# Kernel tuning notes

Hardware: AMD Instinct MI355X
Metric: run time of the kernel (lower is better)

## Reference

```python
import jax, jax.numpy as jnp
import numpy as np

HIDDEN = 768
NUM_HEADS = 12
HEAD_SIZE = HIDDEN // NUM_HEADS
LN_EPS = 1e-12


def setup_inputs() -> dict:
    key = jax.random.key(0)
    ks = jax.random.split(key, 10)
    B, S, H = 32, 512, HIDDEN
    std = 1.0 / np.sqrt(H)
    inp = {
        "x": jax.random.normal(ks[0], (B, S, H), dtype=jnp.float32),
        "additive_attention_mask": jnp.zeros((B, 1, 1, S), dtype=jnp.float32),
        "Wq": jax.random.normal(ks[1], (H, H), dtype=jnp.float32) * std,
        "bq": jax.random.normal(ks[2], (H,), dtype=jnp.float32) * 0.02,
        "Wk": jax.random.normal(ks[3], (H, H), dtype=jnp.float32) * std,
        "bk": jax.random.normal(ks[4], (H,), dtype=jnp.float32) * 0.02,
        "Wv": jax.random.normal(ks[5], (H, H), dtype=jnp.float32) * std,
        "bv": jax.random.normal(ks[6], (H,), dtype=jnp.float32) * 0.02,
        "Wo": jax.random.normal(ks[7], (H, H), dtype=jnp.float32) * std,
        "bo": jax.random.normal(ks[8], (H,), dtype=jnp.float32) * 0.02,
        "ln_w": jnp.ones((H,), dtype=jnp.float32),
        "ln_b": jnp.zeros((H,), dtype=jnp.float32),
    }
    return inp


def _split_heads(y):
    # (b, s, h) -> (b, n_heads, s, head_size)
    b, s, _ = y.shape
    return y.reshape(b, s, NUM_HEADS, HEAD_SIZE).transpose(0, 2, 1, 3)


def reference(x, additive_attention_mask, Wq, bq, Wk, bk, Wv, bv, Wo, bo, ln_w, ln_b):
    # Linear projections (torch Linear: x @ W.T + b)
    q = _split_heads(x @ Wq.T + bq)  # b n s d
    k = _split_heads(x @ Wk.T + bk)
    v = _split_heads(x @ Wv.T + bv)

    scores = jnp.einsum("bnqd,bnkd->bnqk", q, k) / np.sqrt(HEAD_SIZE)
    scores = scores + additive_attention_mask  # (b,1,1,s) broadcasts
    attn = jax.nn.softmax(scores, axis=-1)

    weighted = jnp.einsum("bnqk,bnkd->bnqd", attn, v)
    b, n, s, d = weighted.shape
    weighted = weighted.transpose(0, 2, 1, 3).reshape(b, s, n * d)
    attn_out = weighted @ Wo.T + bo

    # residual + LayerNorm (dropout is identity in eval)
    y = x + attn_out
    mean = jnp.mean(y, axis=-1, keepdims=True)
    var = jnp.var(y, axis=-1, keepdims=True)
    y = (y - mean) / jnp.sqrt(var + LN_EPS)
    return y * ln_w + ln_b
```

## Files before the change

kernel.cpp:

```cpp
#include <hip/hip_runtime.h>

#define HIDDEN 768
#define NHEAD 12
#define HDIM 64
#define SEQ 512
#define BATCH 32
#define MTOT (BATCH*SEQ)

typedef __attribute__((ext_vector_type(8))) short short8;
typedef __attribute__((ext_vector_type(4))) float f32x4;
typedef __attribute__((ext_vector_type(4))) unsigned short us4;

#define LOG2E 1.44269504088896340736f

__device__ __forceinline__ unsigned short f2bf(float f){
  unsigned u = __builtin_bit_cast(unsigned, f);
  u += 0x7fff + ((u >> 16) & 1);
  return (unsigned short)(u >> 16);
}

__device__ __forceinline__ float bf2f(unsigned short s){
  unsigned u = ((unsigned)s) << 16;
  return __builtin_bit_cast(float, u);
}

__device__ __forceinline__ float fexp2(float x){
  float r;
  asm("v_exp_f32 %0, %1\n\ts_nop 0" : "=v"(r) : "v"(x));
  return r;
}

__device__ __forceinline__ void gload16(unsigned short* lds, const unsigned short* g){
  __builtin_amdgcn_global_load_lds(
      (const __attribute__((address_space(1))) void*)g,
      (__attribute__((address_space(3))) void*)lds, 16, 0, 0);
}

__global__ __launch_bounds__(256) void cvt_kernel(const float* __restrict__ in,
                                                  unsigned short* __restrict__ out, int n4){
  int i = blockIdx.x * blockDim.x + threadIdx.x;
  if (i >= n4) return;
  float4 v = ((const float4*)in)[i];
  ushort4 o;
  o.x = f2bf(v.x); o.y = f2bf(v.y); o.z = f2bf(v.z); o.w = f2bf(v.w);
  ((ushort4*)out)[i] = o;
}

__global__ __launch_bounds__(256) void cvt4_kernel(
    const float* __restrict__ w0, const float* __restrict__ w1,
    const float* __restrict__ w2, const float* __restrict__ w3,
    unsigned short* __restrict__ o0, unsigned short* __restrict__ o1,
    unsigned short* __restrict__ o2, unsigned short* __restrict__ o3){
  const int which = blockIdx.y;
  const float* in = (which==0)?w0:((which==1)?w1:((which==2)?w2:w3));
  unsigned short* out = (which==0)?o0:((which==1)?o1:((which==2)?o2:o3));
  int i = blockIdx.x * blockDim.x + threadIdx.x;
  float4 v = ((const float4*)in)[i];
  ushort4 o;
  o.x = f2bf(v.x); o.y = f2bf(v.y); o.z = f2bf(v.z); o.w = f2bf(v.w);
  ((ushort4*)out)[i] = o;
}


#define STAGE_A(buf, kt_) do { \
    const int kc_ = (kt_)*64; \
    gload16(&sA[buf][(size_t)(tid)*8],      gA + kc_); \
    gload16(&sA[buf][(size_t)(512+tid)*8],  gA + (size_t)64*HIDDEN + kc_); \
    gload16(&sA[buf][(size_t)(1024+tid)*8], gA + (size_t)128*HIDDEN + kc_); \
    gload16(&sA[buf][(size_t)(1536+tid)*8], gA + (size_t)192*HIDDEN + kc_); \
  } while(0)

#define STAGE_B(buf, kt_) do { \
    const int kc_ = (kt_)*64; \
    gload16(&sB[buf][(size_t)(tid)*8],      gB + kc_); \
    gload16(&sB[buf][(size_t)(512+tid)*8],  gB + (size_t)64*HIDDEN + kc_); \
    gload16(&sB[buf][(size_t)(1024+tid)*8], gB + (size_t)128*HIDDEN + kc_); \
  } while(0)

#define GEMM_MAIN() \
  STAGE_A(0, 0); STAGE_B(0, 0); \
  for (int kt = 0; kt < 12; ++kt) { \
    const int c = kt & 1; \
    asm volatile("s_waitcnt vmcnt(0)" ::: "memory"); \
    __builtin_amdgcn_s_barrier(); \
    if (kt < 11) { STAGE_A(c^1, kt+1); STAGE_B(c^1, kt+1); } \
    const unsigned short* bA = sA[c]; \
    const unsigned short* bB = sB[c]; \
    _Pragma("unroll") \
    for (int kk = 0; kk < 2; ++kk) { \
      short8 af[8], bf[3]; \
      _Pragma("unroll") \
      for (int i = 0; i < 8; i++) af[i] = *(const short8*)&bA[aoff[i] ^ (kk*32)]; \
      _Pragma("unroll") \
      for (int i = 0; i < 3; i++) bf[i] = *(const short8*)&bB[boff[i] ^ (kk*32)]; \
      asm volatile("s_waitcnt lgkmcnt(0)" ::: "memory"); \
      __builtin_amdgcn_sched_barrier(0); \
      __builtin_amdgcn_s_setprio(1); \
      _Pragma("unroll") \
      for (int mi2 = 0; mi2 < 8; mi2++) \
        _Pragma("unroll") \
        for (int ni = 0; ni < 3; ni++) \
          acc[mi2][ni] = __builtin_amdgcn_mfma_f32_16x16x32_bf16(af[mi2], bf[ni], acc[mi2][ni], 0, 0, 0); \
      __builtin_amdgcn_s_setprio(0); \
    } \
  }

__global__ __launch_bounds__(512, 2) void qkv_gemm(
    const unsigned short* __restrict__ A,
    const unsigned short* __restrict__ Wq,
    const unsigned short* __restrict__ Wk,
    const unsigned short* __restrict__ Wv,
    const float* __restrict__ bq,
    const float* __restrict__ bk,
    const float* __restrict__ bv,
    unsigned short* __restrict__ Qo,
    unsigned short* __restrict__ Ko,
    unsigned short* __restrict__ VTo)
{
  __shared__ unsigned short sA[2][16384];
  __shared__ unsigned short sB[2][12288];

  const int flat = blockIdx.x;
  const int swzb = (flat & 7) * 96 + (flat >> 3);
  const int mi_ = swzb / 12;
  const int rem = swzb % 12;
  const int mode = rem >> 2;
  const int n0 = (rem & 3) * 192;
  const int m0 = mi_ * 256;
  const unsigned short* W = (mode==0) ? Wq : ((mode==1) ? Wk : Wv);
  const float* bias = (mode==0) ? bq : ((mode==1) ? bk : bv);

  const int tid = threadIdx.x;
  const int lane = tid & 63;
  const int wid = tid >> 6;
  const int wm = wid >> 2, wn = wid & 3;
  const int g = lane >> 4, l16 = lane & 15;

  const int rS = tid >> 3;
  const int gc = (tid & 7) ^ (rS & 7);
  const unsigned short* gA = &A[(size_t)(m0 + rS)*HIDDEN + gc*8];
  const unsigned short* gB = &W[(size_t)(n0 + rS)*HIDDEN + gc*8];

  int aoff[8], boff[3];
  #pragma unroll
  for (int i = 0; i < 8; i++){
    int rm = wm*128 + i*16 + l16;
    aoff[i] = rm*64 + ((g ^ (rm&7)) * 8);
  }
  #pragma unroll
  for (int i = 0; i < 3; i++){
    int rn = wn*48 + i*16 + l16;
    boff[i] = rn*64 + ((g ^ (rn&7)) * 8);
  }

  f32x4 acc[8][3];
  #pragma unroll
  for (int i = 0; i < 8; i++)
    #pragma unroll
    for (int j = 0; j < 3; j++) acc[i][j] = (f32x4){0.f,0.f,0.f,0.f};

  GEMM_MAIN();

  float bvv[3];
  #pragma unroll
  for (int ni = 0; ni < 3; ni++) bvv[ni] = bias[n0 + wn*48 + ni*16 + l16];
  #pragma unroll
  for (int mi2 = 0; mi2 < 8; mi2++) {
    int mbase = m0 + wm*128 + mi2*16 + g*4;
    int b = mbase >> 9, s = mbase & 511;
    #pragma unroll
    for (int ni = 0; ni < 3; ni++) {
      int ncol = n0 + wn*48 + ni*16 + l16;
      int h = ncol >> 6, d = ncol & 63;
      if (mode == 2) {
        us4 v;
        #pragma unroll
        for (int r = 0; r < 4; r++) v[r] = f2bf(acc[mi2][ni][r] + bvv[ni]);
        *(us4*)&VTo[(((size_t)(b*NHEAD)+h)*HDIM + d)*SEQ + s] = v;
      } else {
        #pragma unroll
        for (int r = 0; r < 4; r++) {
          float val = acc[mi2][ni][r] + bvv[ni];
          if (mode == 0) Qo[(((size_t)(b*NHEAD)+h)*SEQ + s + r)*HDIM + d] = f2bf(val * 0.1803368801f);
          else           Ko[(((size_t)(b*NHEAD)+h)*SEQ + s + r)*HDIM + d] = f2bf(val);
        }
      }
    }
  }
}

__global__ __launch_bounds__(512, 2) void proj_gemm(
    const unsigned short* __restrict__ A,
    const unsigned short* __restrict__ W,
    const float* __restrict__ bias,
    unsigned short* __restrict__ Out)
{
  __shared__ unsigned short sA[2][16384];
  __shared__ unsigned short sB[2][12288];

  const int flat = blockIdx.x;
  const int swzb = (flat & 7) * 32 + (flat >> 3);
  const int m0 = (swzb >> 2) * 256;
  const int n0 = (swzb & 3) * 192;

  const int tid = threadIdx.x;
  const int lane = tid & 63;
  const int wid = tid >> 6;
  const int wm = wid >> 2, wn = wid & 3;
  const int g = lane >> 4, l16 = lane & 15;

  const int rS = tid >> 3;
  const int gc = (tid & 7) ^ (rS & 7);
  const unsigned short* gA = &A[(size_t)(m0 + rS)*HIDDEN + gc*8];
  const unsigned short* gB = &W[(size_t)(n0 + rS)*HIDDEN + gc*8];

  int aoff[8], boff[3];
  #pragma unroll
  for (int i = 0; i < 8; i++){
    int rm = wm*128 + i*16 + l16;
    aoff[i] = rm*64 + ((g ^ (rm&7)) * 8);
  }
  #pragma unroll
  for (int i = 0; i < 3; i++){
    int rn = wn*48 + i*16 + l16;
    boff[i] = rn*64 + ((g ^ (rn&7)) * 8);
  }

  f32x4 acc[8][3];
  #pragma unroll
  for (int i = 0; i < 8; i++)
    #pragma unroll
    for (int j = 0; j < 3; j++) acc[i][j] = (f32x4){0.f,0.f,0.f,0.f};

  GEMM_MAIN();

  float bvv[3];
  #pragma unroll
  for (int ni = 0; ni < 3; ni++) bvv[ni] = bias[n0 + wn*48 + ni*16 + l16];
  #pragma unroll
  for (int mi2 = 0; mi2 < 8; mi2++) {
    int mbase = m0 + wm*128 + mi2*16 + g*4;
    #pragma unroll
    for (int ni = 0; ni < 3; ni++) {
      int ncol = n0 + wn*48 + ni*16 + l16;
      #pragma unroll
      for (int r = 0; r < 4; r++)
        Out[(size_t)(mbase + r)*HIDDEN + ncol] = f2bf(acc[mi2][ni][r] + bvv[ni]);
    }
  }
}

__global__ __launch_bounds__(256) void attn_kernel(
    const unsigned short* __restrict__ Q,
    const unsigned short* __restrict__ K,
    const unsigned short* __restrict__ VT,
    const float* __restrict__ mask,
    unsigned short* __restrict__ ctx)
{
  __shared__ unsigned short sK[3][4096];
  __shared__ unsigned short sV[3][4096];
  __shared__ unsigned short P_lds[4*16*68];
  __shared__ float sMask[512];

  const int flat = blockIdx.x;
  const int swzb = (flat & 7) * 192 + (flat >> 3);
  const int qt = swzb & 3;
  const int bh = swzb >> 2;
  const int b = bh / NHEAD, h = bh % NHEAD;
  const int tid = threadIdx.x;
  const int lane = tid & 63;
  const int wid = tid >> 6;
  const int g = lane >> 4, l16 = lane & 15;
  const int qbase = qt*128 + wid*32;

  const int rS = tid >> 3;
  const int cbS = (tid & 7) ^ (rS & 7);
  const size_t khb = (size_t)bh * SEQ;
  const unsigned short* gK  = &K[(khb + rS)*HDIM + cbS*8];
  const unsigned short* gK2 = gK + (size_t)32*HDIM;
  const unsigned short* gV  = &VT[((size_t)bh*HDIM + rS)*SEQ + cbS*8];
  const unsigned short* gV2 = gV + (size_t)32*SEQ;

  sMask[tid]       = mask[b*SEQ + tid] * LOG2E;
  sMask[tid + 256] = mask[b*SEQ + tid + 256] * LOG2E;

  short8 aQ0[2], aQ1[2];
  #pragma unroll
  for (int q16 = 0; q16 < 2; q16++){
    const unsigned short* qp = &Q[(khb + qbase + q16*16 + l16)*HDIM];
    aQ0[q16] = *(const short8*)&qp[g*8];
    aQ1[q16] = *(const short8*)&qp[32 + g*8];
  }

  int off[4];
  {
    const int sw = (g ^ (l16 & 7)) * 8;
    #pragma unroll
    for (int i = 0; i < 4; i++) off[i] = (i*16 + l16)*64 + sw;
  }

  float l_r[2][4];
  f32x4 o_acc[2][4];
  #pragma unroll
  for (int q16 = 0; q16 < 2; q16++){
    #pragma unroll
    for (int r = 0; r < 4; r++) l_r[q16][r] = 0.f;
    #pragma unroll
    for (int dt = 0; dt < 4; dt++) o_acc[q16][dt] = (f32x4){0.f,0.f,0.f,0.f};
  }

#define KSTAGE(buf_, t_) do { \
    gload16(&sK[buf_][wid*512],        gK  + (size_t)(t_)*64*HDIM); \
    gload16(&sK[buf_][2048 + wid*512], gK2 + (size_t)(t_)*64*HDIM); \
    gload16(&sV[buf_][wid*512],        gV  + (t_)*64); \
    gload16(&sV[buf_][2048 + wid*512], gV2 + (t_)*64); \
  } while(0)

  KSTAGE(0, 0);
  KSTAGE(1, 1);
  asm volatile("s_waitcnt lgkmcnt(0)" ::: "memory");

  int cb = 0;
  for (int kt = 0; kt < 8; ++kt) {
    if (kt < 7) asm volatile("s_waitcnt vmcnt(4)" ::: "memory");
    else        asm volatile("s_waitcnt vmcnt(0)" ::: "memory");
    __builtin_amdgcn_s_barrier();
    __builtin_amdgcn_sched_barrier(0);
    if (kt < 6) { const int sb = (cb == 0) ? 2 : cb - 1; KSTAGE(sb, kt + 2); }
    const unsigned short* bK = sK[cb];
    const unsigned short* bV = sV[cb];
    const int kv0 = kt * 64;

    f32x4 sacc[2][4];
    #pragma unroll
    for (int ct = 0; ct < 4; ++ct) {
      short8 k0 = *(const short8*)&bK[off[ct]];
      short8 k1 = *(const short8*)&bK[off[ct] ^ 32];
      f32x4 s0 = (f32x4){0.f,0.f,0.f,0.f}, s1 = (f32x4){0.f,0.f,0.f,0.f};
      __builtin_amdgcn_s_setprio(1);
      s0 = __builtin_amdgcn_mfma_f32_16x16x32_bf16(aQ0[0], k0, s0, 0, 0, 0);
      s0 = __builtin_amdgcn_mfma_f32_16x16x32_bf16(aQ1[0], k1, s0, 0, 0, 0);
      s1 = __builtin_amdgcn_mfma_f32_16x16x32_bf16(aQ0[1], k0, s1, 0, 0, 0);
      s1 = __builtin_amdgcn_mfma_f32_16x16x32_bf16(aQ1[1], k1, s1, 0, 0, 0);
      __builtin_amdgcn_s_setprio(0);
      float mv = sMask[kv0 + ct*16 + l16];
      sacc[0][ct] = s0 + mv;
      sacc[1][ct] = s1 + mv;
    }

    #pragma unroll
    for (int q16 = 0; q16 < 2; q16++){
      #pragma unroll
      for (int ct = 0; ct < 4; ct++){
        #pragma unroll
        for (int r = 0; r < 4; r++){
          float p = fexp2(sacc[q16][ct][r]);
          l_r[q16][r] += p;
          P_lds[(wid*16 + g*4 + r)*68 + ct*16 + l16] =
              (unsigned short)(__builtin_bit_cast(unsigned, p) >> 16);
        }
      }
      asm volatile("s_waitcnt lgkmcnt(0)" ::: "memory");
      __builtin_amdgcn_sched_barrier(0);
      short8 pa0 = *(const short8*)&P_lds[(wid*16 + l16)*68 + g*8];
      short8 pa1 = *(const short8*)&P_lds[(wid*16 + l16)*68 + 32 + g*8];
      __builtin_amdgcn_s_setprio(1);
      #pragma unroll
      for (int dt = 0; dt < 4; dt++){
        short8 v0 = *(const short8*)&bV[off[dt]];
        short8 v1 = *(const short8*)&bV[off[dt] ^ 32];
        o_acc[q16][dt] = __builtin_amdgcn_mfma_f32_16x16x32_bf16(pa0, v0, o_acc[q16][dt], 0, 0, 0);
        o_acc[q16][dt] = __builtin_amdgcn_mfma_f32_16x16x32_bf16(pa1, v1, o_acc[q16][dt], 0, 0, 0);
      }
      __builtin_amdgcn_s_setprio(0);
    }
    cb = (cb == 2) ? 0 : cb + 1;
  }

  #pragma unroll
  for (int q16 = 0; q16 < 2; q16++){
    #pragma unroll
    for (int o = 1; o <= 8; o <<= 1){
      #pragma unroll
      for (int r = 0; r < 4; r++) l_r[q16][r] += __shfl_xor(l_r[q16][r], o);
    }
    float inv[4];
    #pragma unroll
    for (int r = 0; r < 4; r++) inv[r] = 1.f / l_r[q16][r];
    #pragma unroll
    for (int dt = 0; dt < 4; dt++){
      #pragma unroll
      for (int r = 0; r < 4; r++){
        int s = qbase + q16*16 + g*4 + r;
        ctx[((size_t)(b*SEQ + s))*HIDDEN + h*HDIM + dt*16 + l16] = f2bf(o_acc[q16][dt][r] * inv[r]);
      }
    }
  }
#undef KSTAGE
}

__global__ __launch_bounds__(256) void resid_ln(
    const unsigned short* __restrict__ xb, const unsigned short* __restrict__ ao,
    const float* __restrict__ lnw, const float* __restrict__ lnb,
    float* __restrict__ out)
{
  const int row = blockIdx.x*4 + (threadIdx.x >> 6);
  const int lane = threadIdx.x & 63;
  const ushort4* xr = (const ushort4*)&xb[(size_t)row*HIDDEN];
  const ushort4* ar = (const ushort4*)&ao[(size_t)row*HIDDEN];
  float4 y[3];
  float s1 = 0.f, s2 = 0.f;
  #pragma unroll
  for (int j = 0; j < 3; j++){
    ushort4 xv = xr[lane + j*64];
    ushort4 av = ar[lane + j*64];
    float4 v;
    v.x = bf2f(xv.x) + bf2f(av.x); v.y = bf2f(xv.y) + bf2f(av.y);
    v.z = bf2f(xv.z) + bf2f(av.z); v.w = bf2f(xv.w) + bf2f(av.w);
    y[j] = v;
    s1 += v.x + v.y + v.z + v.w;
    s2 += v.x*v.x + v.y*v.y + v.z*v.z + v.w*v.w;
  }
  #pragma unroll
  for (int o = 1; o <= 32; o <<= 1){
    s1 += __shfl_xor(s1, o);
    s2 += __shfl_xor(s2, o);
  }
  float mean = s1 * (1.f/768.f);
  float var = s2 * (1.f/768.f) - mean*mean;
  float rstd = rsqrtf(var + 1e-12f);
  float4* orow = (float4*)&out[(size_t)row*HIDDEN];
  #pragma unroll
  for (int j = 0; j < 3; j++){
    float4 gm = ((const float4*)lnw)[lane + j*64];
    float4 bt = ((const float4*)lnb)[lane + j*64];
    float4 o;
    o.x = (y[j].x - mean)*rstd*gm.x + bt.x;
    o.y = (y[j].y - mean)*rstd*gm.y + bt.y;
    o.z = (y[j].z - mean)*rstd*gm.z + bt.z;
    o.w = (y[j].w - mean)*rstd*gm.w + bt.w;
    orow[lane + j*64] = o;
  }
}

extern "C" void kernel_launch(void* const* d_in, const int* in_sizes, int n_in,
                              void* d_out, int out_size, void* d_ws, size_t ws_size,
                              hipStream_t stream) {
  (void)in_sizes; (void)n_in; (void)out_size; (void)ws_size;
  const float* x    = (const float*)d_in[0];
  const float* mask = (const float*)d_in[1];
  const float* Wq   = (const float*)d_in[2];
  const float* bq   = (const float*)d_in[3];
  const float* Wk   = (const float*)d_in[4];
  const float* bk   = (const float*)d_in[5];
  const float* Wv   = (const float*)d_in[6];
  const float* bv   = (const float*)d_in[7];
  const float* Wo   = (const float*)d_in[8];
  const float* bo   = (const float*)d_in[9];
  const float* lnw  = (const float*)d_in[10];
  const float* lnb  = (const float*)d_in[11];
  float* out = (float*)d_out;

  char* w = (char*)d_ws;
  size_t off = 0;
  auto alloc = [&](size_t bytes) -> char* {
    char* p = w + off; off += (bytes + 255) & ~(size_t)255; return p;
  };
  unsigned short* xb  = (unsigned short*)alloc((size_t)MTOT*HIDDEN*2);
  unsigned short* wqb = (unsigned short*)alloc((size_t)HIDDEN*HIDDEN*2);
  unsigned short* wkb = (unsigned short*)alloc((size_t)HIDDEN*HIDDEN*2);
  unsigned short* wvb = (unsigned short*)alloc((size_t)HIDDEN*HIDDEN*2);
  unsigned short* wob = (unsigned short*)alloc((size_t)HIDDEN*HIDDEN*2);
  unsigned short* qb  = (unsigned short*)alloc((size_t)MTOT*HDIM*NHEAD*2);
  unsigned short* kb  = (unsigned short*)alloc((size_t)MTOT*HDIM*NHEAD*2);
  unsigned short* vtb = (unsigned short*)alloc((size_t)MTOT*HDIM*NHEAD*2);
  unsigned short* ctxb= (unsigned short*)alloc((size_t)MTOT*HIDDEN*2);
  unsigned short* attn_out = qb;

  cvt_kernel<<<dim3(MTOT*HIDDEN/4/256), 256, 0, stream>>>(x, xb, MTOT*HIDDEN/4);
  cvt4_kernel<<<dim3(HIDDEN*HIDDEN/4/256, 4), 256, 0, stream>>>(Wq, Wk, Wv, Wo, wqb, wkb, wvb, wob);

  qkv_gemm<<<dim3(768), 512, 0, stream>>>(xb, wqb, wkb, wvb, bq, bk, bv, qb, kb, vtb);

  attn_kernel<<<dim3(1536), 256, 0, stream>>>(qb, kb, vtb, mask, ctxb);

  proj_gemm<<<dim3(256), 512, 0, stream>>>(ctxb, wob, bo, attn_out);

  resid_ln<<<dim3(MTOT/4), 256, 0, stream>>>(xb, attn_out, lnw, lnb, out);
}
```

Measured before the change: 192.7 us.

## Use 8-wave attention blocks sharing K/V tiles, double-buffered; simplify GEMM sync

The attention kernel now runs 512-thread blocks, each covering 256 queries. The number of blocks is halved, so each K/V tile loaded into LDS is reused by twice as many waves. Staging is split so waves 0-3 load K and waves 4-7 load V, and the pipeline goes from triple to double buffering, waiting on vmcnt(0) every iteration. Separately, the GEMM main loop swaps its explicit waitcnt, barrier, sched_barrier and setprio hints for a plain __syncthreads, which may lose the hand-tuned overlap between loads and MFMAs.

```diff
diff --git a/kernel.cpp b/kernel.cpp
--- a/kernel.cpp
+++ b/kernel.cpp
@@ -81,8 +81,7 @@
   STAGE_A(0, 0); STAGE_B(0, 0); \
   for (int kt = 0; kt < 12; ++kt) { \
     const int c = kt & 1; \
-    asm volatile("s_waitcnt vmcnt(0)" ::: "memory"); \
-    __builtin_amdgcn_s_barrier(); \
+    __syncthreads(); \
     if (kt < 11) { STAGE_A(c^1, kt+1); STAGE_B(c^1, kt+1); } \
     const unsigned short* bA = sA[c]; \
     const unsigned short* bB = sB[c]; \
@@ -93,15 +92,11 @@
       for (int i = 0; i < 8; i++) af[i] = *(const short8*)&bA[aoff[i] ^ (kk*32)]; \
       _Pragma("unroll") \
       for (int i = 0; i < 3; i++) bf[i] = *(const short8*)&bB[boff[i] ^ (kk*32)]; \
-      asm volatile("s_waitcnt lgkmcnt(0)" ::: "memory"); \
-      __builtin_amdgcn_sched_barrier(0); \
-      __builtin_amdgcn_s_setprio(1); \
       _Pragma("unroll") \
       for (int mi2 = 0; mi2 < 8; mi2++) \
         _Pragma("unroll") \
         for (int ni = 0; ni < 3; ni++) \
           acc[mi2][ni] = __builtin_amdgcn_mfma_f32_16x16x32_bf16(af[mi2], bf[ni], acc[mi2][ni], 0, 0, 0); \
-      __builtin_amdgcn_s_setprio(0); \
     } \
   }
 
@@ -250,39 +245,38 @@
   }
 }
 
-__global__ __launch_bounds__(256) void attn_kernel(
+__global__ __launch_bounds__(512) void attn_kernel(
     const unsigned short* __restrict__ Q,
     const unsigned short* __restrict__ K,
     const unsigned short* __restrict__ VT,
     const float* __restrict__ mask,
     unsigned short* __restrict__ ctx)
 {
-  __shared__ unsigned short sK[3][4096];
-  __shared__ unsigned short sV[3][4096];
-  __shared__ unsigned short P_lds[4*16*68];
+  __shared__ unsigned short sK[2][4096];
+  __shared__ unsigned short sV[2][4096];
+  __shared__ unsigned short P_lds[8*16*68];
   __shared__ float sMask[512];
 
   const int flat = blockIdx.x;
-  const int swzb = (flat & 7) * 192 + (flat >> 3);
-  const int qt = swzb & 3;
-  const int bh = swzb >> 2;
+  const int swzb = (flat & 7) * 96 + (flat >> 3);
+  const int qt = swzb & 1;
+  const int bh = swzb >> 1;
   const int b = bh / NHEAD, h = bh % NHEAD;
   const int tid = threadIdx.x;
   const int lane = tid & 63;
   const int wid = tid >> 6;
   const int g = lane >> 4, l16 = lane & 15;
-  const int qbase = qt*128 + wid*32;
-
-  const int rS = tid >> 3;
-  const int cbS = (tid & 7) ^ (rS & 7);
+  const int qbase = qt*256 + wid*32;
+
+  const int srow = ((wid & 3) << 4) + (lane >> 3);
+  const int schunk = (lane & 7) ^ (srow & 7);
   const size_t khb = (size_t)bh * SEQ;
-  const unsigned short* gK  = &K[(khb + rS)*HDIM + cbS*8];
-  const unsigned short* gK2 = gK + (size_t)32*HDIM;
-  const unsigned short* gV  = &VT[((size_t)bh*HDIM + rS)*SEQ + cbS*8];
-  const unsigned short* gV2 = gV + (size_t)32*SEQ;
-
-  sMask[tid]       = mask[b*SEQ + tid] * LOG2E;
-  sMask[tid + 256] = mask[b*SEQ + tid + 256] * LOG2E;
+  const unsigned short* gKs  = &K[(khb + srow)*HDIM + schunk*8];
+  const unsigned short* gKs2 = gKs + (size_t)8*HDIM;
+  const unsigned short* gVs  = &VT[((size_t)bh*HDIM + srow)*SEQ + schunk*8];
+  const unsigned short* gVs2 = gVs + (size_t)8*SEQ;
+
+  sMask[tid] = mask[b*SEQ + tid] * LOG2E;
 
   short8 aQ0[2], aQ1[2];
   #pragma unroll
@@ -310,23 +304,24 @@
   }
 
 #define KSTAGE(buf_, t_) do { \
-    gload16(&sK[buf_][wid*512],        gK  + (size_t)(t_)*64*HDIM); \
-    gload16(&sK[buf_][2048 + wid*512], gK2 + (size_t)(t_)*64*HDIM); \
-    gload16(&sV[buf_][wid*512],        gV  + (t_)*64); \
-    gload16(&sV[buf_][2048 + wid*512], gV2 + (t_)*64); \
+    if (wid < 4) { \
+      gload16(&sK[buf_][(size_t)((wid & 3) << 10)],       gKs  + (size_t)(t_)*64*HDIM); \
+      gload16(&sK[buf_][(size_t)((wid & 3) << 10) + 512], gKs2 + (size_t)(t_)*64*HDIM); \
+    } else { \
+      gload16(&sV[buf_][(size_t)((wid & 3) << 10)],       gVs  + (t_)*64); \
+      gload16(&sV[buf_][(size_t)((wid & 3) << 10) + 512], gVs2 + (t_)*64); \
+    } \
   } while(0)
 
   KSTAGE(0, 0);
-  KSTAGE(1, 1);
   asm volatile("s_waitcnt lgkmcnt(0)" ::: "memory");
 
   int cb = 0;
   for (int kt = 0; kt < 8; ++kt) {
-    if (kt < 7) asm volatile("s_waitcnt vmcnt(4)" ::: "memory");
-    else        asm volatile("s_waitcnt vmcnt(0)" ::: "memory");
+    asm volatile("s_waitcnt vmcnt(0)" ::: "memory");
     __builtin_amdgcn_s_barrier();
     __builtin_amdgcn_sched_barrier(0);
-    if (kt < 6) { const int sb = (cb == 0) ? 2 : cb - 1; KSTAGE(sb, kt + 2); }
+    if (kt < 7) KSTAGE(cb ^ 1, kt + 1);
     const unsigned short* bK = sK[cb];
     const unsigned short* bV = sV[cb];
     const int kv0 = kt * 64;
@@ -374,7 +369,7 @@
       }
       __builtin_amdgcn_s_setprio(0);
     }
-    cb = (cb == 2) ? 0 : cb + 1;
+    cb ^= 1;
   }
 
   #pragma unroll
@@ -482,7 +477,7 @@
 
   qkv_gemm<<<dim3(768), 512, 0, stream>>>(xb, wqb, wkb, wvb, bq, bk, bv, qb, kb, vtb);
 
-  attn_kernel<<<dim3(1536), 256, 0, stream>>>(qb, kb, vtb, mask, ctxb);
+  attn_kernel<<<dim3(768), 512, 0, stream>>>(qb, kb, vtb, mask, ctxb);
 
   proj_gemm<<<dim3(256), 512, 0, stream>>>(ctxb, wob, bo, attn_out);
 
```

Result: faster. 187.1 us (-2.9%).
